# Performance work log

Hardware: AMD Instinct MI355X
Metric: run time of the kernel (lower is better)

The kernel has to match this reference:

```python
import jax, jax.numpy as jnp
import numpy as np
from jax import lax


def setup_inputs() -> dict:
    key = jax.random.key(0)
    ks = jax.random.split(key, 7)
    B, T, I, H = 256, 1024, 128, 256
    s = 0.05  # keep gates out of deep saturation
    return {
        "x": jax.random.normal(ks[0], (B, T, I), dtype=jnp.float32),
        "h0": jax.random.normal(ks[1], (1, B, H), dtype=jnp.float32),
        "c0": jax.random.normal(ks[2], (1, B, H), dtype=jnp.float32),
        "w_ih": jax.random.normal(ks[3], (4 * H, I), dtype=jnp.float32) * s,
        "w_hh": jax.random.normal(ks[4], (4 * H, H), dtype=jnp.float32) * s,
        "b_ih": jax.random.normal(ks[5], (4 * H,), dtype=jnp.float32) * s,
        "b_hh": jax.random.normal(ks[6], (4 * H,), dtype=jnp.float32) * s,
    }


def reference(x, h0, c0, w_ih, w_hh, b_ih, b_hh):
    # Single-layer LSTM over full sequence, returning final hidden state hn [1, B, H].
    H = h0.shape[-1]
    # Precompute input contribution for all timesteps: [T, B, 4H]
    gx = jnp.einsum('bti,gi->tbg', x, w_ih) + (b_ih + b_hh)

    def step(carry, gx_t):
        h, c = carry                      # [B, H], [B, H]
        g = gx_t + h @ w_hh.T             # [B, 4H]
        i_g, f_g, g_g, o_g = jnp.split(g, 4, axis=-1)  # PyTorch gate order i,f,g,o
        i = jax.nn.sigmoid(i_g)
        f = jax.nn.sigmoid(f_g)
        gg = jnp.tanh(g_g)
        o = jax.nn.sigmoid(o_g)
        c_new = f * c + i * gg
        h_new = o * jnp.tanh(c_new)
        return (h_new, c_new), None

    (hT, cT), _ = lax.scan(step, (h0[0], c0[0]), gx)
    return hT[None]  # [1, B, H]
```

## Files before the change

kernel.cpp:

```cpp
#include <hip/hip_runtime.h>

typedef __attribute__((ext_vector_type(8))) short   short8;
typedef __attribute__((ext_vector_type(4))) float   float4_;
typedef __attribute__((ext_vector_type(4))) unsigned int uint4_;

#define WPACK_OFF   0
#define WPACK_BYTES 786432
#define HBUF_OFF    786432
#define HBUF_BYTES  524288
#define BIAS_OFF    (HBUF_OFF + HBUF_BYTES)

#define SLOT_ULL 16384
#define SENT_ULL 0xFFFFFFFFFFFFFFFFull

__device__ __forceinline__ unsigned short f2bf(float f) {
  unsigned int u = __float_as_uint(f);
  u += 0x7fffu + ((u >> 16) & 1u);
  return (unsigned short)(u >> 16);
}

__global__ void pack_w(const float* __restrict__ w_ih,
                       const float* __restrict__ w_hh,
                       unsigned short* __restrict__ wpack) {
  int idx = blockIdx.x * blockDim.x + threadIdx.x;
  if (idx >= 49152) return;
  int lane = idx & 63;
  int r1 = idx >> 6;
  int kt = r1 % 12;
  int r2 = r1 / 12;
  int g  = r2 & 3;
  int r3 = r2 >> 2;
  int wv = r3 & 3;
  int s4 = r3 >> 2;
  int row = g * 256 + s4 * 64 + wv * 16 + (lane & 15);
  int q = lane >> 4;
  short8 o;
#pragma unroll
  for (int j = 0; j < 8; ++j) {
    int kk = kt * 32 + q * 8 + j;
    float v = (kt < 8) ? w_hh[row * 256 + kk]
                       : w_ih[row * 128 + (kk - 256)];
    o[j] = (short)f2bf(v);
  }
  *(short8*)(wpack + (size_t)idx * 8) = o;
}

__global__ void init_hb(const float* __restrict__ h0,
                        const float* __restrict__ b_ih,
                        const float* __restrict__ b_hh,
                        unsigned long long* __restrict__ hbuf,
                        float* __restrict__ bias) {
  int idx = blockIdx.x * blockDim.x + threadIdx.x;
  if (idx < 16384) {
    unsigned long long v = 0;
#pragma unroll
    for (int e = 0; e < 4; ++e)
      v |= (unsigned long long)f2bf(h0[idx * 4 + e]) << (16 * e);
    hbuf[idx] = v;
  } else if (idx < 65536) {
    hbuf[idx] = SENT_ULL;
  } else if (idx < 66560) {
    int j = idx - 65536;
    bias[j] = b_ih[j] + b_hh[j];
  }
}

__device__ __forceinline__ float sigm_(float v) {
  return 1.f / (1.f + __expf(-v));
}
__device__ __forceinline__ float tanh_(float v) {
  return 1.f - 2.f / (__expf(2.f * v) + 1.f);
}

__global__ __launch_bounds__(256, 1) void lstm_main(
    const float* __restrict__ x, const float* __restrict__ c0,
    const unsigned short* __restrict__ wpack, const float* __restrict__ bias,
    unsigned long long* hbuf, float* __restrict__ out) {

  const int tid  = threadIdx.x;
  const int wv   = tid >> 6;
  const int lane = tid & 63;
  const int q    = lane >> 4;
  const int bl   = lane & 15;

  const int id  = blockIdx.x;
  const int s4  = id >> 4;
  const int grp = id & 15;

  const int bg = grp * 16 + bl;

  short8 wf[48];
  {
    const unsigned short* base =
        wpack + ((size_t)((s4 * 4 + wv) * 48) * 64 + lane) * 8;
#pragma unroll
    for (int f = 0; f < 48; ++f)
      wf[f] = *(const short8*)(base + (size_t)f * 512);
  }
#pragma unroll
  for (int f = 0; f < 48; ++f)
    asm volatile("" : "+v"(wf[f]));

  float4_ bia[4];
#pragma unroll
  for (int g = 0; g < 4; ++g)
    bia[g] = *(const float4_*)(bias + g * 256 + s4 * 64 + wv * 16 + q * 4);

  float4_ cst = *(const float4_*)(c0 + (size_t)bg * 256 + s4 * 64 + wv * 16 + q * 4);

  const size_t my_ull = (size_t)bg * 64 + s4 * 16 + wv * 4 + q;
  unsigned long long hull = hbuf[my_ull];

  const float* xb = x + (size_t)bg * 131072 + wv * 32 + q * 8;
  float4_ xr0 = *(const float4_*)(xb);
  float4_ xr1 = *(const float4_*)(xb + 4);

  __shared__ uint4_ hbf[12][64];

  float4_ hf;

#pragma unroll 1
  for (int t = 0; t < 1024; ++t) {
    {
      short8 xf;
#pragma unroll
      for (int e = 0; e < 4; ++e) {
        xf[e]     = (short)f2bf(xr0[e]);
        xf[e + 4] = (short)f2bf(xr1[e]);
      }
      *(short8*)&hbf[8 + wv][lane] = xf;
    }
    ((unsigned long long*)&hbf[2 * s4 + (wv >> 1)]
                              [(2 * (wv & 1) + (q >> 1)) * 16 + bl])[q & 1] = hull;

    if (wv != s4) {
      unsigned long long* hb =
          hbuf + (size_t)(t & 3) * SLOT_ULL + (size_t)bg * 64 + wv * 16 + q * 2;
      unsigned long long p0, p1, p2, p3;
      for (;;) {
        p0 = __hip_atomic_load(hb,     __ATOMIC_RELAXED, __HIP_MEMORY_SCOPE_AGENT);
        p1 = __hip_atomic_load(hb + 1, __ATOMIC_RELAXED, __HIP_MEMORY_SCOPE_AGENT);
        p2 = __hip_atomic_load(hb + 8, __ATOMIC_RELAXED, __HIP_MEMORY_SCOPE_AGENT);
        p3 = __hip_atomic_load(hb + 9, __ATOMIC_RELAXED, __HIP_MEMORY_SCOPE_AGENT);
        bool ok = ((unsigned short)p0 != 0xFFFFu) & ((unsigned short)p1 != 0xFFFFu)
                & ((unsigned short)p2 != 0xFFFFu) & ((unsigned short)p3 != 0xFFFFu);
        if (__all(ok)) break;
        __builtin_amdgcn_s_sleep(1);
      }
      asm volatile("" ::: "memory");
      union { unsigned long long u[2]; uint4_ v; } u0, u1;
      u0.u[0] = p0; u0.u[1] = p1;
      u1.u[0] = p2; u1.u[1] = p3;
      hbf[2 * wv][lane]     = u0.v;
      hbf[2 * wv + 1][lane] = u1.v;
    }
    __syncthreads();

    {
      int tn = (t < 1023) ? (t + 1) : 1023;
      xr0 = *(const float4_*)(xb + (size_t)tn * 128);
      xr1 = *(const float4_*)(xb + (size_t)tn * 128 + 4);
    }

    float4_ acc[4];
#pragma unroll
    for (int g = 0; g < 4; ++g) acc[g] = bia[g];

#pragma unroll
    for (int kt = 0; kt < 12; ++kt) {
      short8 bf = *(const short8*)&hbf[kt][lane];
#pragma unroll
      for (int g = 0; g < 4; ++g)
        acc[g] = __builtin_amdgcn_mfma_f32_16x16x32_bf16(wf[g * 12 + kt], bf, acc[g], 0, 0, 0);
    }

    if (t > 0) {
      unsigned long long* rp =
          hbuf + (size_t)((t - 1) & 3) * SLOT_ULL + my_ull;
      __hip_atomic_store(rp, SENT_ULL, __ATOMIC_RELAXED, __HIP_MEMORY_SCOPE_AGENT);
    }
    {
      unsigned long long nh = 0;
#pragma unroll
      for (int r = 0; r < 4; ++r) {
        float iv = sigm_(acc[0][r]);
        float fv = sigm_(acc[1][r]);
        float gv = tanh_(acc[2][r]);
        float ov = sigm_(acc[3][r]);
        float cv = fv * cst[r] + iv * gv;
        cst[r] = cv;
        float hv = ov * tanh_(cv);
        hf[r] = hv;
        nh |= (unsigned long long)f2bf(hv) << (16 * r);
      }
      hull = nh;
      unsigned long long* dst =
          hbuf + (size_t)((t + 1) & 3) * SLOT_ULL + my_ull;
      __hip_atomic_store(dst, hull, __ATOMIC_RELAXED, __HIP_MEMORY_SCOPE_AGENT);
    }
    __syncthreads();
  }

  *(float4_*)(out + (size_t)bg * 256 + s4 * 64 + wv * 16 + q * 4) = hf;
}

extern "C" void kernel_launch(void* const* d_in, const int* in_sizes, int n_in,
                              void* d_out, int out_size, void* d_ws, size_t ws_size,
                              hipStream_t stream) {
  (void)in_sizes; (void)n_in; (void)out_size; (void)ws_size;
  const float* x    = (const float*)d_in[0];
  const float* h0   = (const float*)d_in[1];
  const float* c0   = (const float*)d_in[2];
  const float* w_ih = (const float*)d_in[3];
  const float* w_hh = (const float*)d_in[4];
  const float* b_ih = (const float*)d_in[5];
  const float* b_hh = (const float*)d_in[6];

  char* ws = (char*)d_ws;
  unsigned short*     wpack = (unsigned short*)(ws + WPACK_OFF);
  unsigned long long* hbuf  = (unsigned long long*)(ws + HBUF_OFF);
  float*              bias  = (float*)(ws + BIAS_OFF);

  pack_w<<<192, 256, 0, stream>>>(w_ih, w_hh, wpack);
  init_hb<<<260, 256, 0, stream>>>(h0, b_ih, b_hh, hbuf, bias);
  lstm_main<<<64, 256, 0, stream>>>(x, c0, wpack, bias, hbuf, (float*)d_out);
}
```

Baseline: 2.389 ms.

## Drop LDS staging and block barriers; poll global h directly per wave

Each wave now reads the full previous hidden state from the global exchange buffer straight into MFMA operands, removing the shared-memory staging and both __syncthreads per step. The input projection for step t+1 is computed off the critical path after publishing h, with x prefetched two steps ahead. The hbuf layout is changed to be group-major so the per-wave polling loads are contiguous, and slot reset is moved earlier. In exchange, every wave polls 16 global words (more global traffic), and it adds an explicit vmcnt wait before the publish store.

```diff
diff --git a/kernel.cpp b/kernel.cpp
--- a/kernel.cpp
+++ b/kernel.cpp
@@ -2,7 +2,6 @@
 
 typedef __attribute__((ext_vector_type(8))) short   short8;
 typedef __attribute__((ext_vector_type(4))) float   float4_;
-typedef __attribute__((ext_vector_type(4))) unsigned int uint4_;
 
 #define WPACK_OFF   0
 #define WPACK_BYTES 786432
@@ -52,10 +51,15 @@
                         float* __restrict__ bias) {
   int idx = blockIdx.x * blockDim.x + threadIdx.x;
   if (idx < 16384) {
+    int grp = idx >> 10;
+    int rem = idx & 1023;
+    int nu  = rem >> 4;
+    int bw  = rem & 15;
+    int b   = grp * 16 + bw;
     unsigned long long v = 0;
 #pragma unroll
     for (int e = 0; e < 4; ++e)
-      v |= (unsigned long long)f2bf(h0[idx * 4 + e]) << (16 * e);
+      v |= (unsigned long long)f2bf(h0[b * 256 + nu * 4 + e]) << (16 * e);
     hbuf[idx] = v;
   } else if (idx < 65536) {
     hbuf[idx] = SENT_ULL;
@@ -108,97 +112,130 @@
 
   float4_ cst = *(const float4_*)(c0 + (size_t)bg * 256 + s4 * 64 + wv * 16 + q * 4);
 
-  const size_t my_ull = (size_t)bg * 64 + s4 * 16 + wv * 4 + q;
-  unsigned long long hull = hbuf[my_ull];
-
-  const float* xb = x + (size_t)bg * 131072 + wv * 32 + q * 8;
-  float4_ xr0 = *(const float4_*)(xb);
-  float4_ xr1 = *(const float4_*)(xb + 4);
-
-  __shared__ uint4_ hbf[12][64];
+  const float* xrow = x + (size_t)bg * 131072 + q * 8;
+  float4_ xr[8];
+#pragma unroll
+  for (int kx = 0; kx < 4; ++kx) {
+    xr[kx * 2]     = *(const float4_*)(xrow + kx * 32);
+    xr[kx * 2 + 1] = *(const float4_*)(xrow + kx * 32 + 4);
+  }
+
+  float4_ accx[4];
+  {
+    short8 xf[4];
+#pragma unroll
+    for (int kx = 0; kx < 4; ++kx) {
+      short8 v;
+#pragma unroll
+      for (int e = 0; e < 4; ++e) {
+        v[e]     = (short)f2bf(xr[kx * 2][e]);
+        v[e + 4] = (short)f2bf(xr[kx * 2 + 1][e]);
+      }
+      xf[kx] = v;
+    }
+#pragma unroll
+    for (int g = 0; g < 4; ++g) accx[g] = bia[g];
+#pragma unroll
+    for (int kx = 0; kx < 4; ++kx)
+#pragma unroll
+      for (int g = 0; g < 4; ++g)
+        accx[g] = __builtin_amdgcn_mfma_f32_16x16x32_bf16(wf[g * 12 + 8 + kx], xf[kx], accx[g], 0, 0, 0);
+  }
+#pragma unroll
+  for (int kx = 0; kx < 4; ++kx) {
+    xr[kx * 2]     = *(const float4_*)(xrow + 128 + kx * 32);
+    xr[kx * 2 + 1] = *(const float4_*)(xrow + 128 + kx * 32 + 4);
+  }
+
+  const int    poff   = q * 32 + bl;
+  const size_t gbase  = (size_t)grp * 1024;
+  const size_t my_off = gbase + (size_t)(s4 * 16 + wv * 4 + q) * 16 + bl;
 
   float4_ hf;
 
 #pragma unroll 1
   for (int t = 0; t < 1024; ++t) {
+    unsigned long long p[16];
     {
-      short8 xf;
-#pragma unroll
-      for (int e = 0; e < 4; ++e) {
-        xf[e]     = (short)f2bf(xr0[e]);
-        xf[e + 4] = (short)f2bf(xr1[e]);
-      }
-      *(short8*)&hbf[8 + wv][lane] = xf;
-    }
-    ((unsigned long long*)&hbf[2 * s4 + (wv >> 1)]
-                              [(2 * (wv & 1) + (q >> 1)) * 16 + bl])[q & 1] = hull;
-
-    if (wv != s4) {
-      unsigned long long* hb =
-          hbuf + (size_t)(t & 3) * SLOT_ULL + (size_t)bg * 64 + wv * 16 + q * 2;
-      unsigned long long p0, p1, p2, p3;
+      unsigned long long* hb = hbuf + (size_t)(t & 3) * SLOT_ULL + gbase + poff;
       for (;;) {
-        p0 = __hip_atomic_load(hb,     __ATOMIC_RELAXED, __HIP_MEMORY_SCOPE_AGENT);
-        p1 = __hip_atomic_load(hb + 1, __ATOMIC_RELAXED, __HIP_MEMORY_SCOPE_AGENT);
-        p2 = __hip_atomic_load(hb + 8, __ATOMIC_RELAXED, __HIP_MEMORY_SCOPE_AGENT);
-        p3 = __hip_atomic_load(hb + 9, __ATOMIC_RELAXED, __HIP_MEMORY_SCOPE_AGENT);
-        bool ok = ((unsigned short)p0 != 0xFFFFu) & ((unsigned short)p1 != 0xFFFFu)
-                & ((unsigned short)p2 != 0xFFFFu) & ((unsigned short)p3 != 0xFFFFu);
+#pragma unroll
+        for (int kt = 0; kt < 8; ++kt) {
+          p[kt * 2]     = __hip_atomic_load(hb + kt * 128,      __ATOMIC_RELAXED, __HIP_MEMORY_SCOPE_AGENT);
+          p[kt * 2 + 1] = __hip_atomic_load(hb + kt * 128 + 16, __ATOMIC_RELAXED, __HIP_MEMORY_SCOPE_AGENT);
+        }
+        bool ok = true;
+#pragma unroll
+        for (int i = 0; i < 16; ++i)
+          ok &= ((unsigned short)p[i] != 0xFFFFu);
         if (__all(ok)) break;
         __builtin_amdgcn_s_sleep(1);
       }
-      asm volatile("" ::: "memory");
-      union { unsigned long long u[2]; uint4_ v; } u0, u1;
-      u0.u[0] = p0; u0.u[1] = p1;
-      u1.u[0] = p2; u1.u[1] = p3;
-      hbf[2 * wv][lane]     = u0.v;
-      hbf[2 * wv + 1][lane] = u1.v;
-    }
-    __syncthreads();
+    }
+    asm volatile("" ::: "memory");
+
+    __hip_atomic_store(hbuf + (size_t)((t + 2) & 3) * SLOT_ULL + my_off,
+                       SENT_ULL, __ATOMIC_RELAXED, __HIP_MEMORY_SCOPE_AGENT);
+
+    float4_ acc[4];
+#pragma unroll
+    for (int g = 0; g < 4; ++g) acc[g] = accx[g];
+
+#pragma unroll
+    for (int kt = 0; kt < 8; ++kt) {
+      union { unsigned long long u[2]; short8 v; } uu;
+      uu.u[0] = p[kt * 2];
+      uu.u[1] = p[kt * 2 + 1];
+#pragma unroll
+      for (int g = 0; g < 4; ++g)
+        acc[g] = __builtin_amdgcn_mfma_f32_16x16x32_bf16(wf[g * 12 + kt], uu.v, acc[g], 0, 0, 0);
+    }
+
+    unsigned long long nh = 0;
+#pragma unroll
+    for (int r = 0; r < 4; ++r) {
+      float iv = sigm_(acc[0][r]);
+      float fv = sigm_(acc[1][r]);
+      float gv = tanh_(acc[2][r]);
+      float ov = sigm_(acc[3][r]);
+      float cv = fv * cst[r] + iv * gv;
+      cst[r] = cv;
+      float hv = ov * tanh_(cv);
+      hf[r] = hv;
+      nh |= (unsigned long long)f2bf(hv) << (16 * r);
+    }
+
+    asm volatile("s_waitcnt vmcnt(0)" ::: "memory");
+    __hip_atomic_store(hbuf + (size_t)((t + 1) & 3) * SLOT_ULL + my_off,
+                       nh, __ATOMIC_RELAXED, __HIP_MEMORY_SCOPE_AGENT);
 
     {
-      int tn = (t < 1023) ? (t + 1) : 1023;
-      xr0 = *(const float4_*)(xb + (size_t)tn * 128);
-      xr1 = *(const float4_*)(xb + (size_t)tn * 128 + 4);
-    }
-
-    float4_ acc[4];
-#pragma unroll
-    for (int g = 0; g < 4; ++g) acc[g] = bia[g];
-
-#pragma unroll
-    for (int kt = 0; kt < 12; ++kt) {
-      short8 bf = *(const short8*)&hbf[kt][lane];
-#pragma unroll
-      for (int g = 0; g < 4; ++g)
-        acc[g] = __builtin_amdgcn_mfma_f32_16x16x32_bf16(wf[g * 12 + kt], bf, acc[g], 0, 0, 0);
-    }
-
-    if (t > 0) {
-      unsigned long long* rp =
-          hbuf + (size_t)((t - 1) & 3) * SLOT_ULL + my_ull;
-      __hip_atomic_store(rp, SENT_ULL, __ATOMIC_RELAXED, __HIP_MEMORY_SCOPE_AGENT);
-    }
-    {
-      unsigned long long nh = 0;
-#pragma unroll
-      for (int r = 0; r < 4; ++r) {
-        float iv = sigm_(acc[0][r]);
-        float fv = sigm_(acc[1][r]);
-        float gv = tanh_(acc[2][r]);
-        float ov = sigm_(acc[3][r]);
-        float cv = fv * cst[r] + iv * gv;
-        cst[r] = cv;
-        float hv = ov * tanh_(cv);
-        hf[r] = hv;
-        nh |= (unsigned long long)f2bf(hv) << (16 * r);
-      }
-      hull = nh;
-      unsigned long long* dst =
-          hbuf + (size_t)((t + 1) & 3) * SLOT_ULL + my_ull;
-      __hip_atomic_store(dst, hull, __ATOMIC_RELAXED, __HIP_MEMORY_SCOPE_AGENT);
-    }
-    __syncthreads();
+      short8 xf[4];
+#pragma unroll
+      for (int kx = 0; kx < 4; ++kx) {
+        short8 v;
+#pragma unroll
+        for (int e = 0; e < 4; ++e) {
+          v[e]     = (short)f2bf(xr[kx * 2][e]);
+          v[e + 4] = (short)f2bf(xr[kx * 2 + 1][e]);
+        }
+        xf[kx] = v;
+      }
+#pragma unroll
+      for (int g = 0; g < 4; ++g) accx[g] = bia[g];
+#pragma unroll
+      for (int kx = 0; kx < 4; ++kx)
+#pragma unroll
+        for (int g = 0; g < 4; ++g)
+          accx[g] = __builtin_amdgcn_mfma_f32_16x16x32_bf16(wf[g * 12 + 8 + kx], xf[kx], accx[g], 0, 0, 0);
+      int tn = (t < 1022) ? (t + 2) : 1023;
+      const float* xp = xrow + (size_t)tn * 128;
+#pragma unroll
+      for (int kx = 0; kx < 4; ++kx) {
+        xr[kx * 2]     = *(const float4_*)(xp + kx * 32);
+        xr[kx * 2 + 1] = *(const float4_*)(xp + kx * 32 + 4);
+      }
+    }
   }
 
   *(float4_*)(out + (size_t)bg * 256 + s4 * 64 + wv * 16 + q * 4) = hf;
```

After: 3.393 ms. +42.0%, slower.
